# Kernel optimization log

Hardware: AMD Instinct MI355X
Metric: run time of the kernel (lower is better)

## Reference

```python
import math
import jax, jax.numpy as jnp
import numpy as np

B, N, D = 16, 4096, 256
N_CAT, N_TPC, N_VPT, N_SP = 16, 8, 4, 16
N_TYPE = N_CAT * N_TPC          # 128
N_VAR = N_TYPE * N_VPT          # 512
THRESH = 0.1
MASK_VAL = jnp.finfo(jnp.float32).min / 2


def _linear(x, w, b):
    # torch nn.Linear: y = x @ W^T + b, W: (out, in)
    return x @ w.T + b


def _level(codes, proj_w, proj_b, K, X, mask, tau):
    """One codebook level: attention of codes over tokens.
    codes: (M, d). Returns H:(B,M,d), w_raw:(B,M)."""
    Q = _linear(codes, proj_w, proj_b)                       # (M, d)
    attn = jnp.einsum('md,bnd->bmn', Q, K) / math.sqrt(D)    # (B, M, N)
    attn = jnp.where(mask[:, None, :], attn, MASK_VAL)
    attn = jnp.clip(attn, -50.0, 50.0)
    G = jnp.nan_to_num(jax.nn.softmax(attn, axis=-1))        # (B, M, N)
    H = jnp.einsum('bmn,bnd->bmd', G, X)                     # (B, M, d)
    w_raw = jnp.linalg.norm(H, axis=-1) / tau                # (B, M)
    return H, w_raw


def _sparsify(w, thr):
    ws = jnp.where(w > thr, w, 0.0)
    return ws / (ws.sum(axis=-1, keepdims=True) + 1e-8)


def _forward(X, positions, category_codes, type_codes, variant_codes,
             spatial_codes, log_tau, cat_w, cat_b, type_w, type_b,
             var_w, var_b, sp_w, sp_b, k_w, k_b, g1_w, g1_b, g2_w, g2_b,
             out_w, out_b, ln_g, ln_b, level_weights, mask):
    tau = jnp.clip(jnp.exp(log_tau[0]) + 0.1, 0.1, 2.0)
    K = _linear(X, k_w, k_b)                                 # (B, N, d)

    # Level 0: category
    H_cat, w_cat_raw = _level(category_codes, cat_w, cat_b, K, X, mask, tau)
    w_cat = jax.nn.softmax(w_cat_raw, axis=-1)
    w_cat_sp = _sparsify(w_cat, THRESH)

    # Level 1: type, gated by category selection
    H_type, w_type_raw = _level(type_codes.reshape(-1, D), type_w, type_b,
                                K, X, mask, tau)
    w_t = (w_type_raw.reshape(-1, N_CAT, N_TPC) * w_cat_sp[:, :, None]
           ).reshape(-1, N_TYPE)
    w_type = jax.nn.softmax(w_t, axis=-1)
    w_type_sp = _sparsify(w_type, THRESH / 2)

    # Level 2: variant, gated by type selection
    H_var, w_var_raw = _level(variant_codes.reshape(-1, D), var_w, var_b,
                              K, X, mask, tau)
    w_type_exp = jnp.repeat(w_type_sp, N_VPT, axis=-1)       # (B, 512)
    w_var = jax.nn.softmax(w_var_raw * w_type_exp, axis=-1)
    w_var_sp = _sparsify(w_var, THRESH / 4)

    # Spatial level (independent)
    H_sp, w_sp_raw = _level(spatial_codes, sp_w, sp_b, K, X, mask, tau)
    w_sp = jax.nn.softmax(w_sp_raw, axis=-1)
    w_sp_sp = _sparsify(w_sp, THRESH)

    z_cat = jnp.einsum('bm,bmd->bd', w_cat_sp, H_cat)
    z_type = jnp.einsum('bm,bmd->bd', w_type_sp, H_type)
    z_var = jnp.einsum('bm,bmd->bd', w_var_sp, H_var)
    z_spatial = jnp.einsum('bm,bmd->bd', w_sp_sp, H_sp)

    # Position gating of category summary
    mask_f = mask.astype(X.dtype)[:, :, None]
    pos_pooled = (positions * mask_f).sum(1) / jnp.maximum(mask_f.sum(1), 1.0)
    gate_in = jnp.concatenate([z_cat, pos_pooled], axis=-1)  # (B, 2d)
    h = jax.nn.gelu(_linear(gate_in, g1_w, g1_b), approximate=False)
    pos_gate = jax.nn.sigmoid(_linear(h, g2_w, g2_b))
    z_cat = z_cat * pos_gate

    # Learned level combine + gated output projection
    lw = jax.nn.softmax(level_weights)
    z = (lw[0] * z_cat + lw[1] * z_type + lw[2] * z_var + lw[3] * z_spatial)
    z = _linear(z, out_w, out_b)
    mu = z.mean(-1, keepdims=True)
    var = z.var(-1, keepdims=True)
    z = (z - mu) / jnp.sqrt(var + 1e-5) * ln_g + ln_b
    return z


def setup_inputs() -> dict:
    key = jax.random.key(0)
    ks = jax.random.split(key, 32)
    s = 1.0 / math.sqrt(D)
    inp = {
        'X': jax.random.normal(ks[0], (B, N, D), jnp.float32),
        'positions': jax.random.normal(ks[1], (B, N, D), jnp.float32),
        'category_codes': jax.random.normal(ks[2], (N_CAT, D)) * 0.02,
        'type_codes': jax.random.normal(ks[3], (N_CAT, N_TPC, D)) * 0.02,
        'variant_codes': jax.random.normal(ks[4], (N_CAT, N_TPC, N_VPT, D)) * 0.02,
        'spatial_codes': jax.random.normal(ks[5], (N_SP, D)) * 0.02,
        'log_tau': jnp.zeros((1,), jnp.float32),
        'cat_w': jax.random.normal(ks[6], (D, D)) * s,
        'cat_b': jnp.zeros((D,)),
        'type_w': jax.random.normal(ks[7], (D, D)) * s,
        'type_b': jnp.zeros((D,)),
        'var_w': jax.random.normal(ks[8], (D, D)) * s,
        'var_b': jnp.zeros((D,)),
        'sp_w': jax.random.normal(ks[9], (D, D)) * s,
        'sp_b': jnp.zeros((D,)),
        'k_w': jax.random.normal(ks[10], (D, D)) * s,
        'k_b': jnp.zeros((D,)),
        'g1_w': jax.random.normal(ks[11], (D, 2 * D)) * s,
        'g1_b': jnp.zeros((D,)),
        'g2_w': jax.random.normal(ks[12], (D, D)) * s,
        'g2_b': jnp.zeros((D,)),
        'out_w': jax.random.normal(ks[13], (D, D)) * s,
        'out_b': jnp.zeros((D,)),
        'ln_g': jnp.ones((D,)),
        'ln_b': jnp.zeros((D,)),
        'level_weights': jnp.ones((4,)) / 4.0,
        'mask': jnp.ones((B, N), jnp.bool_),
    }
    return inp


def reference(X, positions, category_codes, type_codes, variant_codes,
              spatial_codes, log_tau, cat_w, cat_b, type_w, type_b,
              var_w, var_b, sp_w, sp_b, k_w, k_b, g1_w, g1_b, g2_w, g2_b,
              out_w, out_b, ln_g, ln_b, level_weights, mask):
    return _forward(X, positions, category_codes, type_codes, variant_codes,
                    spatial_codes, log_tau, cat_w, cat_b, type_w, type_b,
                    var_w, var_b, sp_w, sp_b, k_w, k_b, g1_w, g1_b,
                    g2_w, g2_b, out_w, out_b, ln_g, ln_b, level_weights, mask)
```

## Files before the change

kernel.cpp:

```cpp
#include <hip/hip_runtime.h>


#define DEV static __device__ __forceinline__

typedef short bf16x8 __attribute__((ext_vector_type(8)));
typedef float f32x4 __attribute__((ext_vector_type(4)));
typedef unsigned short u16x8 __attribute__((ext_vector_type(8)));

DEV float bf2f(unsigned short u) {
  return __uint_as_float(((unsigned int)u) << 16);
}
DEV unsigned short f2bf(float f) {
  unsigned int x = __float_as_uint(f);
  unsigned int r = (x + 0x7fffu + ((x >> 16) & 1u)) >> 16;
  return (unsigned short)r;
}

DEV void gl2lds16(const void* g, void* l) {
  __builtin_amdgcn_global_load_lds(
      (const __attribute__((address_space(1))) unsigned int*)g,
      (__attribute__((address_space(3))) unsigned int*)l, 16, 0, 0);
}

DEV bf16x8 pack8(const float4 a, const float4 b) {
  bf16x8 r;
  r[0] = (short)f2bf(a.x); r[1] = (short)f2bf(a.y);
  r[2] = (short)f2bf(a.z); r[3] = (short)f2bf(a.w);
  r[4] = (short)f2bf(b.x); r[5] = (short)f2bf(b.y);
  r[6] = (short)f2bf(b.z); r[7] = (short)f2bf(b.w);
  return r;
}

DEV size_t pk_off(int rt, int ks) { return ((size_t)rt * 8 + ks) * 512; }

__global__ __launch_bounds__(256) void fused_pre(
    const float* __restrict__ X, const float* __restrict__ k_w,
    const float* __restrict__ k_b, unsigned short* __restrict__ Kp,
    unsigned short* __restrict__ XTp, const float* __restrict__ positions,
    const unsigned char* __restrict__ mask, float* __restrict__ pacc,
    float* __restrict__ cnt, const float* __restrict__ cat_codes,
    const float* __restrict__ type_codes, const float* __restrict__ var_codes,
    const float* __restrict__ sp_codes, const float* __restrict__ cat_w,
    const float* __restrict__ cat_b, const float* __restrict__ type_w,
    const float* __restrict__ type_b, const float* __restrict__ var_w,
    const float* __restrict__ var_b, const float* __restrict__ sp_w,
    const float* __restrict__ sp_b, unsigned short* __restrict__ Qp) {
  __shared__ __align__(16) char smem[36864];
  const int g = blockIdx.x;
  const int t = threadIdx.x;

  if (g < 1024) {
    unsigned short* As = (unsigned short*)smem;
    unsigned short* Bs = (unsigned short*)(smem + 18432);
    const int m0 = (g >> 1) * 128, c0 = (g & 1) * 128;
    const int l = t & 63, w = t >> 6;
    const int wm = (w & 1) * 64, wn = (w >> 1) * 64;
    const f32x4 zero = {0.f, 0.f, 0.f, 0.f};
    f32x4 acc[4][4];
#pragma unroll
    for (int i = 0; i < 4; ++i)
#pragma unroll
      for (int j = 0; j < 4; ++j) acc[i][j] = zero;
    const int rr = t >> 3, cc = (t & 7) * 8;
    for (int kc = 0; kc < 256; kc += 64) {
      __syncthreads();
#pragma unroll
      for (int p = 0; p < 4; ++p) {
        const int r = p * 32 + rr;
        const float* xs = &X[(size_t)(m0 + r) * 256 + kc + cc];
        const float4 a0 = *(const float4*)&xs[0];
        const float4 a1 = *(const float4*)&xs[4];
        *(bf16x8*)&As[r * 72 + cc] = pack8(a0, a1);
        const float* wsrc = &k_w[(size_t)(c0 + r) * 256 + kc + cc];
        const float4 b0 = *(const float4*)&wsrc[0];
        const float4 b1 = *(const float4*)&wsrc[4];
        *(bf16x8*)&Bs[r * 72 + cc] = pack8(b0, b1);
      }
      __syncthreads();
#pragma unroll
      for (int ks = 0; ks < 2; ++ks) {
        const int koff = ks * 32 + ((l >> 4) & 3) * 8;
        bf16x8 a[4], b[4];
#pragma unroll
        for (int f = 0; f < 4; ++f)
          a[f] = *(const bf16x8*)&As[(wm + f * 16 + (l & 15)) * 72 + koff];
#pragma unroll
        for (int f = 0; f < 4; ++f)
          b[f] = *(const bf16x8*)&Bs[(wn + f * 16 + (l & 15)) * 72 + koff];
#pragma unroll
        for (int i = 0; i < 4; ++i)
#pragma unroll
          for (int j = 0; j < 4; ++j)
            acc[i][j] = __builtin_amdgcn_mfma_f32_16x16x32_bf16(
                a[i], b[j], acc[i][j], 0, 0, 0);
      }
    }
    const int q = (l >> 4) & 3;
#pragma unroll
    for (int j = 0; j < 4; ++j) {
      const int c = c0 + wn + j * 16 + (l & 15);
      const float bv = k_b[c];
#pragma unroll
      for (int i = 0; i < 4; ++i) {
        const int mrow = m0 + wm + i * 16 + q * 4;
#pragma unroll
        for (int r = 0; r < 4; ++r) {
          const int m = mrow + r;
          Kp[pk_off(m >> 4, c >> 5) + ((m & 15) + 16 * ((c >> 3) & 3)) * 8 +
             (c & 7)] = f2bf(acc[i][j][r] + bv);
        }
      }
    }
  } else if (g < 5120) {
    float (*Ls)[65] = (float (*)[65])smem;
    const int gg = g - 1024;
    const int b = gg >> 8;
    const int td = (gg >> 6) & 3;
    const int tn = gg & 63;
    const int nl = t >> 2, dp = (t & 3) * 16;
    const float* src =
        X + ((size_t)b * 4096 + tn * 64 + nl) * 256 + td * 64 + dp;
#pragma unroll
    for (int v = 0; v < 4; ++v) {
      const float4 x = *(const float4*)&src[v * 4];
      Ls[nl][dp + v * 4 + 0] = x.x;
      Ls[nl][dp + v * 4 + 1] = x.y;
      Ls[nl][dp + v * 4 + 2] = x.z;
      Ls[nl][dp + v * 4 + 3] = x.w;
    }
    __syncthreads();
    const int dl = t >> 2, np = (t & 3) * 16;
    u16x8 h0, h1;
#pragma unroll
    for (int j = 0; j < 8; ++j) h0[j] = f2bf(Ls[np + j][dl]);
#pragma unroll
    for (int j = 0; j < 8; ++j) h1[j] = f2bf(Ls[np + 8 + j][dl]);
    const int d = td * 64 + dl;
    const int n0g = tn * 64 + np;
    const int n1g = n0g + 8;
    unsigned short* dst = XTp + (size_t)b * 1048576;
    const size_t o0 = (((size_t)(d >> 4) * 128) + (n0g >> 5)) * 512 +
                      ((d & 15) + 16 * ((n0g >> 3) & 3)) * 8;
    const size_t o1 = (((size_t)(d >> 4) * 128) + (n1g >> 5)) * 512 +
                      ((d & 15) + 16 * ((n1g >> 3) & 3)) * 8;
    *(u16x8*)&dst[o0] = h0;
    *(u16x8*)&dst[o1] = h1;
  } else if (g < 5632) {
    float4* red4 = (float4*)smem;
    float* redc = (float*)(smem + 4096);
    const int gg = g - 5120;
    const int b = gg >> 5, seg = gg & 31;
    const int dg = t & 63;
    const int nl = t >> 6;
    const int n0 = seg * 128;
    float4 acc = make_float4(0.f, 0.f, 0.f, 0.f);
    float c = 0.f;
    const float* pb = positions + (size_t)b * 4096 * 256;
    for (int j = 0; j < 32; ++j) {
      const int n = n0 + j * 4 + nl;
      const float mf = mask[(size_t)b * 4096 + n] ? 1.f : 0.f;
      const float4 v = *(const float4*)&pb[(size_t)n * 256 + dg * 4];
      acc.x = fmaf(mf, v.x, acc.x);
      acc.y = fmaf(mf, v.y, acc.y);
      acc.z = fmaf(mf, v.z, acc.z);
      acc.w = fmaf(mf, v.w, acc.w);
      c += mf;
    }
    red4[t] = acc;
    if (dg == 0) redc[nl] = c;
    __syncthreads();
    if (t < 64) {
      float4 s = red4[t];
      const float4 s1 = red4[t + 64], s2 = red4[t + 128], s3 = red4[t + 192];
      s.x += s1.x + s2.x + s3.x;
      s.y += s1.y + s2.y + s3.y;
      s.z += s1.z + s2.z + s3.z;
      s.w += s1.w + s2.w + s3.w;
      float* pa = pacc + b * 256 + t * 4;
      atomicAdd(pa + 0, s.x);
      atomicAdd(pa + 1, s.y);
      atomicAdd(pa + 2, s.z);
      atomicAdd(pa + 3, s.w);
      if (t == 0) atomicAdd(&cnt[b], redc[0] + redc[1] + redc[2] + redc[3]);
    }
  } else {
    float* xs = (float*)smem;
    const int m = g - 5632;
    const size_t off = pk_off(m >> 4, t >> 5) +
                       ((m & 15) + 16 * ((t >> 3) & 3)) * 8 + (t & 7);
    if (m >= 672) {
      Qp[off] = 0;
      return;
    }
    const float* code;
    const float* W;
    const float* bias;
    if (m < 16)       { code = cat_codes  + m * 256;         W = cat_w;  bias = cat_b; }
    else if (m < 144) { code = type_codes + (m - 16) * 256;  W = type_w; bias = type_b; }
    else if (m < 656) { code = var_codes  + (m - 144) * 256; W = var_w;  bias = var_b; }
    else              { code = sp_codes   + (m - 656) * 256; W = sp_w;   bias = sp_b; }
    xs[t] = code[t];
    __syncthreads();
    float a = bias[t];
    const float* wr = W + (size_t)t * 256;
    for (int k = 0; k < 256; k += 4) {
      const float4 w = *(const float4*)&wr[k];
      a = fmaf(w.x, xs[k], a);
      a = fmaf(w.y, xs[k + 1], a);
      a = fmaf(w.z, xs[k + 2], a);
      a = fmaf(w.w, xs[k + 3], a);
    }
    Qp[off] = f2bf(a);
  }
}

__global__ __launch_bounds__(256, 2) void attn_fused(
    const unsigned short* __restrict__ Qp, const unsigned short* __restrict__ Kp,
    const unsigned short* __restrict__ XTp,
    const unsigned char* __restrict__ mask, float* __restrict__ H2,
    float* __restrict__ lsum2) {
  __shared__ __align__(16) unsigned short Ks[2][16384];
  __shared__ __align__(16) unsigned short Plds[64 * 72];
  __shared__ unsigned char msk[2048];
  const int combo = blockIdx.x;
  const int m0 = blockIdx.y * 64;
  const int b = combo >> 1;
  const int nsl = combo & 1;
  const int nbase = nsl * 2048;
  const int t = threadIdx.x, l = t & 63, w = t >> 6;
  const int l15 = l & 15, q = l >> 4;
  ((uint2*)msk)[t] = ((const uint2*)(mask + (size_t)b * 4096 + nbase))[t];
  const int mt_g = (m0 >> 4) + w;
  bf16x8 qf[8];
#pragma unroll
  for (int ks = 0; ks < 8; ++ks)
    qf[ks] = *(const bf16x8*)&Qp[pk_off(mt_g, ks) + l * 8];
  const f32x4 zero = {0.f, 0.f, 0.f, 0.f};
  f32x4 accO[4][4];
#pragma unroll
  for (int i = 0; i < 4; ++i)
#pragma unroll
    for (int j = 0; j < 4; ++j) accO[i][j] = zero;
  f32x4 rs = zero;
  const unsigned short* XTb = XTp + (size_t)b * 1048576;
  const unsigned short* Kchunk0 = Kp + ((size_t)b * 256 + (nbase >> 4)) * 4096;
#pragma unroll
  for (int i = 0; i < 8; ++i)
    gl2lds16(Kchunk0 + (w * 8 + i) * 512 + l * 8, &Ks[0][(w * 8 + i) * 512]);
  for (int c = 0; c < 32; ++c) {
    const int cur = c & 1;
    __syncthreads();
    const int nst0 = (nbase >> 5) + c * 2;
    bf16x8 xf[2][4];
#pragma unroll
    for (int ks2 = 0; ks2 < 2; ++ks2)
#pragma unroll
      for (int dj = 0; dj < 4; ++dj)
        xf[ks2][dj] = *(const bf16x8*)&XTb[((size_t)(4 * w + dj) * 128 +
                                            nst0 + ks2) * 512 + l * 8];
    f32x4 accS[4];
#pragma unroll
    for (int f = 0; f < 4; ++f) accS[f] = zero;
#pragma unroll
    for (int ks = 0; ks < 8; ++ks) {
      bf16x8 kf[4];
#pragma unroll
      for (int f = 0; f < 4; ++f)
        kf[f] = *(const bf16x8*)&Ks[cur][(f * 8 + ks) * 512 + l * 8];
#pragma unroll
      for (int f = 0; f < 4; ++f)
        accS[f] = __builtin_amdgcn_mfma_f32_16x16x32_bf16(qf[ks], kf[f],
                                                          accS[f], 0, 0, 0);
    }
#pragma unroll
    for (int f = 0; f < 4; ++f) {
      const bool mk = msk[c * 64 + f * 16 + l15] != 0;
#pragma unroll
      for (int r = 0; r < 4; ++r) {
        float s = accS[f][r] * 0.0625f;
        s = fminf(fmaxf(s, -50.f), 50.f);
        if (!mk) s = -50.f;
        const float e = __expf(s);
        Plds[(w * 16 + q * 4 + r) * 72 + f * 16 + l15] = f2bf(e);
        rs[r] += e;
      }
    }
    __syncthreads();
    if (c < 31) {
      const unsigned short* src = Kchunk0 + (size_t)(c + 1) * 16384;
      unsigned short* dst = &Ks[1 - cur][0];
#pragma unroll
      for (int i = 0; i < 8; ++i)
        gl2lds16(src + (w * 8 + i) * 512 + l * 8, dst + (w * 8 + i) * 512);
    }
#pragma unroll
    for (int ks2 = 0; ks2 < 2; ++ks2) {
      bf16x8 pf[4];
#pragma unroll
      for (int mt = 0; mt < 4; ++mt)
        pf[mt] = *(const bf16x8*)&Plds[(mt * 16 + l15) * 72 + ks2 * 32 + q * 8];
#pragma unroll
      for (int mt = 0; mt < 4; ++mt)
#pragma unroll
        for (int dj = 0; dj < 4; ++dj)
          accO[mt][dj] = __builtin_amdgcn_mfma_f32_16x16x32_bf16(
              pf[mt], xf[ks2][dj], accO[mt][dj], 0, 0, 0);
    }
  }
  float* lpart = lsum2 + (size_t)(nsl * 16 + b) * 672;
#pragma unroll
  for (int r = 0; r < 4; ++r) {
    float v = rs[r];
    v += __shfl_xor(v, 1, 64);
    v += __shfl_xor(v, 2, 64);
    v += __shfl_xor(v, 4, 64);
    v += __shfl_xor(v, 8, 64);
    const int m = m0 + w * 16 + q * 4 + r;
    if (l15 == 0 && m < 672) lpart[m] = v;
  }
  float* Hpart = H2 + (size_t)(nsl * 16 + b) * 672 * 256;
#pragma unroll
  for (int mt = 0; mt < 4; ++mt) {
    const int mbase = m0 + mt * 16 + q * 4;
#pragma unroll
    for (int dj = 0; dj < 4; ++dj) {
      const int d = w * 64 + dj * 16 + l15;
#pragma unroll
      for (int r = 0; r < 4; ++r) {
        const int m = mbase + r;
        if (m < 672) Hpart[(size_t)m * 256 + d] = accO[mt][dj][r];
      }
    }
  }
}

__global__ __launch_bounds__(256) void hnorm_kern(
    const float* __restrict__ H2, const float* __restrict__ lsum2,
    const float* __restrict__ log_tau, float* __restrict__ H,
    float* __restrict__ lsum, float* __restrict__ wraw) {
  const int b = blockIdx.x, j = blockIdx.y;
  const int t = threadIdx.x, l = t & 63, w = t >> 6;
  const int m = j * 4 + w;
  const size_t r0 = ((size_t)b * 672 + m) * 256;
  const size_t r1 = ((size_t)(16 + b) * 672 + m) * 256;
  const float4 v0 = *(const float4*)&H2[r0 + l * 4];
  const float4 v1 = *(const float4*)&H2[r1 + l * 4];
  float4 v;
  v.x = v0.x + v1.x; v.y = v0.y + v1.y;
  v.z = v0.z + v1.z; v.w = v0.w + v1.w;
  *(float4*)&H[r0 + l * 4] = v;
  float ss = v.x * v.x + v.y * v.y + v.z * v.z + v.w * v.w;
#pragma unroll
  for (int s = 1; s < 64; s <<= 1) ss += __shfl_xor(ss, s, 64);
  if (l == 0) {
    const float lt = lsum2[b * 672 + m] + lsum2[(16 + b) * 672 + m];
    const float tau = fminf(fmaxf(expf(log_tau[0]) + 0.1f, 0.1f), 2.0f);
    lsum[b * 672 + m] = lt;
    wraw[b * 672 + m] = sqrtf(ss) / (lt * tau);
  }
}

DEV float wave_max(float v) {
#pragma unroll
  for (int m = 1; m < 64; m <<= 1) v = fmaxf(v, __shfl_xor(v, m, 64));
  return v;
}
DEV float wave_sum(float v) {
#pragma unroll
  for (int m = 1; m < 64; m <<= 1) v += __shfl_xor(v, m, 64);
  return v;
}

__global__ __launch_bounds__(256) void combine_kern(
    const float* __restrict__ wraw, const float* __restrict__ lsum,
    const float* __restrict__ H, float* __restrict__ zbuf) {
  const int b = blockIdx.x, j = blockIdx.y, t = threadIdx.x, l = t & 63;
  __shared__ float wr[672];
  __shared__ float wsp[672];
  for (int i = t; i < 672; i += 256) wr[i] = wraw[b * 672 + i];
  __syncthreads();
  {
    const float v = (l < 16) ? wr[l] : -1e30f;
    const float mx = wave_max(v);
    const float e = (l < 16) ? expf(wr[l] - mx) : 0.f;
    const float s = wave_sum(e);
    float w = e / s;
    w = (w > 0.1f) ? w : 0.f;
    const float s2 = wave_sum(w);
    if (l < 16) wsp[l] = w / (s2 + 1e-8f);
  }
  __syncthreads();
  {
    const float L0 = wr[16 + l] * wsp[l >> 3];
    const float L1 = wr[16 + 64 + l] * wsp[(64 + l) >> 3];
    const float mx = wave_max(fmaxf(L0, L1));
    const float e0 = expf(L0 - mx), e1 = expf(L1 - mx);
    const float s = wave_sum(e0 + e1);
    float w0 = e0 / s, w1 = e1 / s;
    w0 = (w0 > 0.05f) ? w0 : 0.f;
    w1 = (w1 > 0.05f) ? w1 : 0.f;
    const float s2 = wave_sum(w0 + w1);
    const float inv2 = 1.f / (s2 + 1e-8f);
    wsp[16 + l] = w0 * inv2;
    wsp[16 + 64 + l] = w1 * inv2;
  }
  __syncthreads();
  {
    float Lv[8];
    float lm = -1e30f;
#pragma unroll
    for (int jj = 0; jj < 8; ++jj) {
      const int i = l * 8 + jj;
      Lv[jj] = wr[144 + i] * wsp[16 + (i >> 2)];
      lm = fmaxf(lm, Lv[jj]);
    }
    const float mx = wave_max(lm);
    float ls = 0.f;
#pragma unroll
    for (int jj = 0; jj < 8; ++jj) {
      Lv[jj] = expf(Lv[jj] - mx);
      ls += Lv[jj];
    }
    const float s = wave_sum(ls);
    const float inv = 1.f / s;
    float ls2 = 0.f;
#pragma unroll
    for (int jj = 0; jj < 8; ++jj) {
      float w = Lv[jj] * inv;
      w = (w > 0.025f) ? w : 0.f;
      Lv[jj] = w;
      ls2 += w;
    }
    const float s2 = wave_sum(ls2);
    const float inv2 = 1.f / (s2 + 1e-8f);
#pragma unroll
    for (int jj = 0; jj < 8; ++jj) wsp[144 + l * 8 + jj] = Lv[jj] * inv2;
  }
  __syncthreads();
  {
    const float v = (l < 16) ? wr[656 + l] : -1e30f;
    const float mx = wave_max(v);
    const float e = (l < 16) ? expf(wr[656 + l] - mx) : 0.f;
    const float s = wave_sum(e);
    float w = e / s;
    w = (w > 0.1f) ? w : 0.f;
    const float s2 = wave_sum(w);
    if (l < 16) wsp[656 + l] = w / (s2 + 1e-8f);
  }
  __syncthreads();
  for (int i = t; i < 672; i += 256) wsp[i] = wsp[i] / lsum[b * 672 + i];
  __syncthreads();
  const float* Hb = H + (size_t)b * 672 * 256 + t;
  const int s0 = j * 84, s1 = s0 + 84;
  const int Llo[4] = {0, 16, 144, 656};
  const int Lhi[4] = {16, 144, 656, 672};
#pragma unroll
  for (int lv = 0; lv < 4; ++lv) {
    const int lo = max(s0, Llo[lv]);
    const int hi = min(s1, Lhi[lv]);
    if (lo >= hi) continue;
    float z = 0.f;
    for (int m = lo; m < hi; ++m)
      z = fmaf(wsp[m], Hb[(size_t)m * 256], z);
    atomicAdd(&zbuf[(b * 4 + lv) * 256 + t], z);
  }
}

__global__ __launch_bounds__(256) void gate_kern(
    const float* __restrict__ zbuf, const float* __restrict__ pacc,
    const float* __restrict__ cnt, const float* __restrict__ g1_w,
    const float* __restrict__ g1_b, const float* __restrict__ g2_w,
    const float* __restrict__ g2_b, const float* __restrict__ out_w,
    const float* __restrict__ out_b, const float* __restrict__ ln_g,
    const float* __restrict__ ln_b, const float* __restrict__ lvlw,
    float* __restrict__ out) {
  const int b = blockIdx.x, t = threadIdx.x;
  __shared__ float gin[512];
  __shared__ float hb[256];
  __shared__ float zc[256];
  __shared__ float red[256];
  const float z0 = zbuf[(b * 4 + 0) * 256 + t];
  gin[t] = z0;
  const float c = fmaxf(cnt[b], 1.0f);
  gin[256 + t] = pacc[b * 256 + t] / c;
  __syncthreads();
  float a = g1_b[t];
  const float* w1 = g1_w + (size_t)t * 512;
  for (int k = 0; k < 512; k += 4) {
    const float4 w = *(const float4*)&w1[k];
    a = fmaf(w.x, gin[k], a);
    a = fmaf(w.y, gin[k + 1], a);
    a = fmaf(w.z, gin[k + 2], a);
    a = fmaf(w.w, gin[k + 3], a);
  }
  const float hg = 0.5f * a * (1.0f + erff(a * 0.7071067811865475f));
  hb[t] = hg;
  __syncthreads();
  float a2 = g2_b[t];
  const float* w2 = g2_w + (size_t)t * 256;
  for (int k = 0; k < 256; k += 4) {
    const float4 w = *(const float4*)&w2[k];
    a2 = fmaf(w.x, hb[k], a2);
    a2 = fmaf(w.y, hb[k + 1], a2);
    a2 = fmaf(w.z, hb[k + 2], a2);
    a2 = fmaf(w.w, hb[k + 3], a2);
  }
  const float pg = 1.0f / (1.0f + expf(-a2));
  const float l0 = lvlw[0], l1 = lvlw[1], l2 = lvlw[2], l3 = lvlw[3];
  const float mx = fmaxf(fmaxf(l0, l1), fmaxf(l2, l3));
  const float e0 = expf(l0 - mx), e1 = expf(l1 - mx);
  const float e2 = expf(l2 - mx), e3 = expf(l3 - mx);
  const float einv = 1.0f / (e0 + e1 + e2 + e3);
  const float zmix = (e0 * z0 * pg + e1 * zbuf[(b * 4 + 1) * 256 + t] +
                      e2 * zbuf[(b * 4 + 2) * 256 + t] +
                      e3 * zbuf[(b * 4 + 3) * 256 + t]) * einv;
  zc[t] = zmix;
  __syncthreads();
  float o = out_b[t];
  const float* wo = out_w + (size_t)t * 256;
  for (int k = 0; k < 256; k += 4) {
    const float4 w = *(const float4*)&wo[k];
    o = fmaf(w.x, zc[k], o);
    o = fmaf(w.y, zc[k + 1], o);
    o = fmaf(w.z, zc[k + 2], o);
    o = fmaf(w.w, zc[k + 3], o);
  }
  red[t] = o;
  __syncthreads();
  for (int s = 128; s > 0; s >>= 1) {
    if (t < s) red[t] += red[t + s];
    __syncthreads();
  }
  const float mu = red[0] / 256.f;
  __syncthreads();
  red[t] = o * o;
  __syncthreads();
  for (int s = 128; s > 0; s >>= 1) {
    if (t < s) red[t] += red[t + s];
    __syncthreads();
  }
  const float var = red[0] / 256.f - mu * mu;
  out[b * 256 + t] = (o - mu) * rsqrtf(var + 1e-5f) * ln_g[t] + ln_b[t];
}

extern "C" void kernel_launch(void* const* d_in, const int* in_sizes, int n_in,
                              void* d_out, int out_size, void* d_ws,
                              size_t ws_size, hipStream_t stream) {
  (void)in_sizes; (void)n_in; (void)out_size; (void)ws_size;
  const float* X          = (const float*)d_in[0];
  const float* positions  = (const float*)d_in[1];
  const float* cat_codes  = (const float*)d_in[2];
  const float* type_codes = (const float*)d_in[3];
  const float* var_codes  = (const float*)d_in[4];
  const float* sp_codes   = (const float*)d_in[5];
  const float* log_tau    = (const float*)d_in[6];
  const float* cat_w      = (const float*)d_in[7];
  const float* cat_b      = (const float*)d_in[8];
  const float* type_w     = (const float*)d_in[9];
  const float* type_b     = (const float*)d_in[10];
  const float* var_w      = (const float*)d_in[11];
  const float* var_b      = (const float*)d_in[12];
  const float* sp_w       = (const float*)d_in[13];
  const float* sp_b       = (const float*)d_in[14];
  const float* k_w        = (const float*)d_in[15];
  const float* k_b        = (const float*)d_in[16];
  const float* g1_w       = (const float*)d_in[17];
  const float* g1_b       = (const float*)d_in[18];
  const float* g2_w       = (const float*)d_in[19];
  const float* g2_b       = (const float*)d_in[20];
  const float* out_w      = (const float*)d_in[21];
  const float* out_b      = (const float*)d_in[22];
  const float* ln_g       = (const float*)d_in[23];
  const float* ln_b       = (const float*)d_in[24];
  const float* lvlw       = (const float*)d_in[25];
  const unsigned char* mask = (const unsigned char*)d_in[26];

  char* ws = (char*)d_ws;
  constexpr size_t O_KP  = 0;
  constexpr size_t O_XT  = 33554432;
  constexpr size_t O_QP  = 67108864;
  constexpr size_t O_H2  = 67469312;
  constexpr size_t O_L2  = 89489408;
  constexpr size_t O_L   = 89575424;
  constexpr size_t O_WR  = 89618432;
  constexpr size_t O_PA  = 89661440;
  constexpr size_t O_CNT = 89677824;
  constexpr size_t O_Z   = 89677888;

  unsigned short* Kp  = (unsigned short*)(ws + O_KP);
  unsigned short* XTp = (unsigned short*)(ws + O_XT);
  unsigned short* Qp  = (unsigned short*)(ws + O_QP);
  float* H2           = (float*)(ws + O_H2);
  float* H            = (float*)(ws + O_KP);
  float* lsum2        = (float*)(ws + O_L2);
  float* lsum         = (float*)(ws + O_L);
  float* wraw         = (float*)(ws + O_WR);
  float* pacc         = (float*)(ws + O_PA);
  float* cnt          = (float*)(ws + O_CNT);
  float* zbuf         = (float*)(ws + O_Z);
  float* out          = (float*)d_out;

  hipMemsetAsync(pacc, 0, 16 * 256 * 4, stream);
  hipMemsetAsync(cnt, 0, 64, stream);
  hipMemsetAsync(zbuf, 0, 16 * 4 * 256 * 4, stream);

  fused_pre<<<dim3(6336), 256, 0, stream>>>(
      X, k_w, k_b, Kp, XTp, positions, mask, pacc, cnt, cat_codes, type_codes,
      var_codes, sp_codes, cat_w, cat_b, type_w, type_b, var_w, var_b, sp_w,
      sp_b, Qp);

  attn_fused<<<dim3(32, 11), 256, 0, stream>>>(Qp, Kp, XTp, mask, H2, lsum2);

  hnorm_kern<<<dim3(16, 168), 256, 0, stream>>>(H2, lsum2, log_tau, H, lsum,
                                                wraw);
  combine_kern<<<dim3(16, 8), 256, 0, stream>>>(wraw, lsum, H, zbuf);
  gate_kern<<<dim3(16), 256, 0, stream>>>(zbuf, pacc, cnt, g1_w, g1_b, g2_w,
                                          g2_b, out_w, out_b, ln_g, ln_b, lvlw,
                                          out);
}
```

Baseline: 395.3 us.

## Fold hnorm into combine and replace atomics and memsets with partial buffers

```diff
diff --git a/kernel.cpp b/kernel.cpp
--- a/kernel.cpp
+++ b/kernel.cpp
@@ -37,8 +37,8 @@
     const float* __restrict__ X, const float* __restrict__ k_w,
     const float* __restrict__ k_b, unsigned short* __restrict__ Kp,
     unsigned short* __restrict__ XTp, const float* __restrict__ positions,
-    const unsigned char* __restrict__ mask, float* __restrict__ pacc,
-    float* __restrict__ cnt, const float* __restrict__ cat_codes,
+    const unsigned char* __restrict__ mask, float* __restrict__ ppart,
+    float* __restrict__ cpart, const float* __restrict__ cat_codes,
     const float* __restrict__ type_codes, const float* __restrict__ var_codes,
     const float* __restrict__ sp_codes, const float* __restrict__ cat_w,
     const float* __restrict__ cat_b, const float* __restrict__ type_w,
@@ -176,12 +176,8 @@
       s.y += s1.y + s2.y + s3.y;
       s.z += s1.z + s2.z + s3.z;
       s.w += s1.w + s2.w + s3.w;
-      float* pa = pacc + b * 256 + t * 4;
-      atomicAdd(pa + 0, s.x);
-      atomicAdd(pa + 1, s.y);
-      atomicAdd(pa + 2, s.z);
-      atomicAdd(pa + 3, s.w);
-      if (t == 0) atomicAdd(&cnt[b], redc[0] + redc[1] + redc[2] + redc[3]);
+      *(float4*)&ppart[(size_t)(b * 32 + seg) * 256 + t * 4] = s;
+      if (t == 0) cpart[b * 32 + seg] = redc[0] + redc[1] + redc[2] + redc[3];
     }
   } else {
     float* xs = (float*)smem;
@@ -334,32 +330,6 @@
   }
 }
 
-__global__ __launch_bounds__(256) void hnorm_kern(
-    const float* __restrict__ H2, const float* __restrict__ lsum2,
-    const float* __restrict__ log_tau, float* __restrict__ H,
-    float* __restrict__ lsum, float* __restrict__ wraw) {
-  const int b = blockIdx.x, j = blockIdx.y;
-  const int t = threadIdx.x, l = t & 63, w = t >> 6;
-  const int m = j * 4 + w;
-  const size_t r0 = ((size_t)b * 672 + m) * 256;
-  const size_t r1 = ((size_t)(16 + b) * 672 + m) * 256;
-  const float4 v0 = *(const float4*)&H2[r0 + l * 4];
-  const float4 v1 = *(const float4*)&H2[r1 + l * 4];
-  float4 v;
-  v.x = v0.x + v1.x; v.y = v0.y + v1.y;
-  v.z = v0.z + v1.z; v.w = v0.w + v1.w;
-  *(float4*)&H[r0 + l * 4] = v;
-  float ss = v.x * v.x + v.y * v.y + v.z * v.z + v.w * v.w;
-#pragma unroll
-  for (int s = 1; s < 64; s <<= 1) ss += __shfl_xor(ss, s, 64);
-  if (l == 0) {
-    const float lt = lsum2[b * 672 + m] + lsum2[(16 + b) * 672 + m];
-    const float tau = fminf(fmaxf(expf(log_tau[0]) + 0.1f, 0.1f), 2.0f);
-    lsum[b * 672 + m] = lt;
-    wraw[b * 672 + m] = sqrtf(ss) / (lt * tau);
-  }
-}
-
 DEV float wave_max(float v) {
 #pragma unroll
   for (int m = 1; m < 64; m <<= 1) v = fmaxf(v, __shfl_xor(v, m, 64));
@@ -372,22 +342,41 @@
 }
 
 __global__ __launch_bounds__(256) void combine_kern(
-    const float* __restrict__ wraw, const float* __restrict__ lsum,
-    const float* __restrict__ H, float* __restrict__ zbuf) {
-  const int b = blockIdx.x, j = blockIdx.y, t = threadIdx.x, l = t & 63;
+    const float* __restrict__ H2, const float* __restrict__ lsum2,
+    const float* __restrict__ log_tau, float* __restrict__ zpart) {
+  const int b = blockIdx.x, j = blockIdx.y, t = threadIdx.x;
+  const int l = t & 63, w = t >> 6;
   __shared__ float wr[672];
   __shared__ float wsp[672];
-  for (int i = t; i < 672; i += 256) wr[i] = wraw[b * 672 + i];
+  __shared__ float linv[672];
+  const float tau = fminf(fmaxf(expf(log_tau[0]) + 0.1f, 0.1f), 2.0f);
+  const float* Ha = H2 + (size_t)b * 672 * 256;
+  const float* Hc = H2 + (size_t)(16 + b) * 672 * 256;
+  for (int m = w; m < 672; m += 4) {
+    const float4 va = *(const float4*)&Ha[(size_t)m * 256 + l * 4];
+    const float4 vb = *(const float4*)&Hc[(size_t)m * 256 + l * 4];
+    const float sx = va.x + vb.x, sy = va.y + vb.y;
+    const float sz = va.z + vb.z, sw = va.w + vb.w;
+    float ss = sx * sx + sy * sy + sz * sz + sw * sw;
+#pragma unroll
+    for (int s = 1; s < 64; s <<= 1) ss += __shfl_xor(ss, s, 64);
+    if (l == 0) {
+      const float lt = lsum2[b * 672 + m] + lsum2[(16 + b) * 672 + m];
+      const float li = 1.0f / lt;
+      wr[m] = sqrtf(ss) * li / tau;
+      linv[m] = li;
+    }
+  }
   __syncthreads();
   {
     const float v = (l < 16) ? wr[l] : -1e30f;
     const float mx = wave_max(v);
     const float e = (l < 16) ? expf(wr[l] - mx) : 0.f;
     const float s = wave_sum(e);
-    float w = e / s;
-    w = (w > 0.1f) ? w : 0.f;
-    const float s2 = wave_sum(w);
-    if (l < 16) wsp[l] = w / (s2 + 1e-8f);
+    float ww = e / s;
+    ww = (ww > 0.1f) ? ww : 0.f;
+    const float s2 = wave_sum(ww);
+    if (l < 16) wsp[l] = ww / (s2 + 1e-8f);
   }
   __syncthreads();
   {
@@ -426,10 +415,10 @@
     float ls2 = 0.f;
 #pragma unroll
     for (int jj = 0; jj < 8; ++jj) {
-      float w = Lv[jj] * inv;
-      w = (w > 0.025f) ? w : 0.f;
-      Lv[jj] = w;
-      ls2 += w;
+      float ww = Lv[jj] * inv;
+      ww = (ww > 0.025f) ? ww : 0.f;
+      Lv[jj] = ww;
+      ls2 += ww;
     }
     const float s2 = wave_sum(ls2);
     const float inv2 = 1.f / (s2 + 1e-8f);
@@ -442,15 +431,14 @@
     const float mx = wave_max(v);
     const float e = (l < 16) ? expf(wr[656 + l] - mx) : 0.f;
     const float s = wave_sum(e);
-    float w = e / s;
-    w = (w > 0.1f) ? w : 0.f;
-    const float s2 = wave_sum(w);
-    if (l < 16) wsp[656 + l] = w / (s2 + 1e-8f);
-  }
-  __syncthreads();
-  for (int i = t; i < 672; i += 256) wsp[i] = wsp[i] / lsum[b * 672 + i];
-  __syncthreads();
-  const float* Hb = H + (size_t)b * 672 * 256 + t;
+    float ww = e / s;
+    ww = (ww > 0.1f) ? ww : 0.f;
+    const float s2 = wave_sum(ww);
+    if (l < 16) wsp[656 + l] = ww / (s2 + 1e-8f);
+  }
+  __syncthreads();
+  for (int i = t; i < 672; i += 256) wsp[i] *= linv[i];
+  __syncthreads();
   const int s0 = j * 84, s1 = s0 + 84;
   const int Llo[4] = {0, 16, 144, 656};
   const int Lhi[4] = {16, 144, 656, 672};
@@ -458,17 +446,16 @@
   for (int lv = 0; lv < 4; ++lv) {
     const int lo = max(s0, Llo[lv]);
     const int hi = min(s1, Lhi[lv]);
-    if (lo >= hi) continue;
     float z = 0.f;
     for (int m = lo; m < hi; ++m)
-      z = fmaf(wsp[m], Hb[(size_t)m * 256], z);
-    atomicAdd(&zbuf[(b * 4 + lv) * 256 + t], z);
+      z = fmaf(wsp[m], Ha[(size_t)m * 256 + t] + Hc[(size_t)m * 256 + t], z);
+    zpart[(((size_t)b * 8 + j) * 4 + lv) * 256 + t] = z;
   }
 }
 
 __global__ __launch_bounds__(256) void gate_kern(
-    const float* __restrict__ zbuf, const float* __restrict__ pacc,
-    const float* __restrict__ cnt, const float* __restrict__ g1_w,
+    const float* __restrict__ zpart, const float* __restrict__ ppart,
+    const float* __restrict__ cpart, const float* __restrict__ g1_w,
     const float* __restrict__ g1_b, const float* __restrict__ g2_w,
     const float* __restrict__ g2_b, const float* __restrict__ out_w,
     const float* __restrict__ out_b, const float* __restrict__ ln_g,
@@ -479,10 +466,23 @@
   __shared__ float hb[256];
   __shared__ float zc[256];
   __shared__ float red[256];
-  const float z0 = zbuf[(b * 4 + 0) * 256 + t];
-  gin[t] = z0;
-  const float c = fmaxf(cnt[b], 1.0f);
-  gin[256 + t] = pacc[b * 256 + t] / c;
+  float zv[4];
+#pragma unroll
+  for (int lv = 0; lv < 4; ++lv) {
+    float z = 0.f;
+#pragma unroll
+    for (int jj = 0; jj < 8; ++jj)
+      z += zpart[(((size_t)b * 8 + jj) * 4 + lv) * 256 + t];
+    zv[lv] = z;
+  }
+  float pa = 0.f, c = 0.f;
+  for (int seg = 0; seg < 32; ++seg) {
+    pa += ppart[(size_t)(b * 32 + seg) * 256 + t];
+    c += cpart[b * 32 + seg];
+  }
+  c = fmaxf(c, 1.0f);
+  gin[t] = zv[0];
+  gin[256 + t] = pa / c;
   __syncthreads();
   float a = g1_b[t];
   const float* w1 = g1_w + (size_t)t * 512;
@@ -511,9 +511,8 @@
   const float e0 = expf(l0 - mx), e1 = expf(l1 - mx);
   const float e2 = expf(l2 - mx), e3 = expf(l3 - mx);
   const float einv = 1.0f / (e0 + e1 + e2 + e3);
-  const float zmix = (e0 * z0 * pg + e1 * zbuf[(b * 4 + 1) * 256 + t] +
-                      e2 * zbuf[(b * 4 + 2) * 256 + t] +
-                      e3 * zbuf[(b * 4 + 3) * 256 + t]) * einv;
+  const float zmix =
+      (e0 * zv[0] * pg + e1 * zv[1] + e2 * zv[2] + e3 * zv[3]) * einv;
   zc[t] = zmix;
   __syncthreads();
   float o = out_b[t];
@@ -581,40 +580,30 @@
   constexpr size_t O_QP  = 67108864;
   constexpr size_t O_H2  = 67469312;
   constexpr size_t O_L2  = 89489408;
-  constexpr size_t O_L   = 89575424;
-  constexpr size_t O_WR  = 89618432;
-  constexpr size_t O_PA  = 89661440;
-  constexpr size_t O_CNT = 89677824;
-  constexpr size_t O_Z   = 89677888;
+  constexpr size_t O_PP  = 89575424;
+  constexpr size_t O_CP  = 90099712;
+  constexpr size_t O_ZP  = 90101760;
 
   unsigned short* Kp  = (unsigned short*)(ws + O_KP);
   unsigned short* XTp = (unsigned short*)(ws + O_XT);
   unsigned short* Qp  = (unsigned short*)(ws + O_QP);
   float* H2           = (float*)(ws + O_H2);
-  float* H            = (float*)(ws + O_KP);
   float* lsum2        = (float*)(ws + O_L2);
-  float* lsum         = (float*)(ws + O_L);
-  float* wraw         = (float*)(ws + O_WR);
-  float* pacc         = (float*)(ws + O_PA);
-  float* cnt          = (float*)(ws + O_CNT);
-  float* zbuf         = (float*)(ws + O_Z);
+  float* ppart        = (float*)(ws + O_PP);
+  float* cpart        = (float*)(ws + O_CP);
+  float* zpart        = (float*)(ws + O_ZP);
   float* out          = (float*)d_out;
 
-  hipMemsetAsync(pacc, 0, 16 * 256 * 4, stream);
-  hipMemsetAsync(cnt, 0, 64, stream);
-  hipMemsetAsync(zbuf, 0, 16 * 4 * 256 * 4, stream);
-
   fused_pre<<<dim3(6336), 256, 0, stream>>>(
-      X, k_w, k_b, Kp, XTp, positions, mask, pacc, cnt, cat_codes, type_codes,
-      var_codes, sp_codes, cat_w, cat_b, type_w, type_b, var_w, var_b, sp_w,
-      sp_b, Qp);
+      X, k_w, k_b, Kp, XTp, positions, mask, ppart, cpart, cat_codes,
+      type_codes, var_codes, sp_codes, cat_w, cat_b, type_w, type_b, var_w,
+      var_b, sp_w, sp_b, Qp);
 
   attn_fused<<<dim3(32, 11), 256, 0, stream>>>(Qp, Kp, XTp, mask, H2, lsum2);
 
-  hnorm_kern<<<dim3(16, 168), 256, 0, stream>>>(H2, lsum2, log_tau, H, lsum,
-                                                wraw);
-  combine_kern<<<dim3(16, 8), 256, 0, stream>>>(wraw, lsum, H, zbuf);
-  gate_kern<<<dim3(16), 256, 0, stream>>>(zbuf, pacc, cnt, g1_w, g1_b, g2_w,
-                                          g2_b, out_w, out_b, ln_g, ln_b, lvlw,
-                                          out);
-}
+  combine_kern<<<dim3(16, 8), 256, 0, stream>>>(H2, lsum2, log_tau, zpart);
+
+  gate_kern<<<dim3(16), 256, 0, stream>>>(zpart, ppart, cpart, g1_w, g1_b,
+                                          g2_w, g2_b, out_w, out_b, ln_g,
+                                          ln_b, lvlw, out);
+}
```

Result: slower. 481.4 us (+21.8%).
